# Optimization experiments

Hardware: AMD Instinct MI355X
Metric: run time of the kernel (lower is better)

## Reference

```python
import jax, jax.numpy as jnp
import numpy as np

DIM = 1028


def setup_inputs() -> dict:
    key = jax.random.key(0)
    ks = jax.random.split(key, 11)
    B, N = 8, 2048
    s = 0.02
    x = jax.random.normal(ks[0], (B, N, DIM), dtype=jnp.float32)
    Wq = jax.random.normal(ks[1], (DIM, DIM), dtype=jnp.float32) * s
    bq = jax.random.normal(ks[2], (DIM,), dtype=jnp.float32) * s
    Wk = jax.random.normal(ks[3], (DIM, DIM), dtype=jnp.float32) * s
    bk = jax.random.normal(ks[4], (DIM,), dtype=jnp.float32) * s
    Wv = jax.random.normal(ks[5], (DIM, DIM), dtype=jnp.float32) * s
    bv = jax.random.normal(ks[6], (DIM,), dtype=jnp.float32) * s
    We = jax.random.normal(ks[7], (4 * DIM, DIM), dtype=jnp.float32) * s
    be = jax.random.normal(ks[8], (4 * DIM,), dtype=jnp.float32) * s
    Wo = jax.random.normal(ks[9], (DIM, 4 * DIM), dtype=jnp.float32) * s
    bo = jax.random.normal(ks[10], (DIM,), dtype=jnp.float32) * s
    return {"x": x, "Wq": Wq, "bq": bq, "Wk": Wk, "bk": bk, "Wv": Wv,
            "bv": bv, "We": We, "be": be, "Wo": Wo, "bo": bo}


def reference(x, Wq, bq, Wk, bk, Wv, bv, We, be, Wo, bo):
    # x: [B, N, D]. torch Linear weight is [out, in] -> x @ W.T + b
    q = jnp.einsum('bnd,ed->bne', x, Wq) + bq
    k = jnp.einsum('bnd,ed->bne', x, Wk) + bk
    v = jnp.einsum('bnd,ed->bne', x, Wv) + bv
    scores = jnp.einsum('bqd,bkd->bqk', q, k) / jnp.sqrt(jnp.float32(DIM))
    w = jax.nn.softmax(scores, axis=-1)          # [B, N, N]
    attn = jnp.einsum('bqk,bkd->bqd', w, v)      # [B, N, D]
    h = jax.nn.gelu(jnp.einsum('bnd,hd->bnh', attn, We) + be, approximate=False)
    out = jnp.einsum('bnh,dh->bnd', h, Wo) + bo
    return out + x
```

## Files before the change

kernel.cpp:

```cpp
#include <hip/hip_runtime.h>
#include <hip/hip_bf16.h>
#include <cstdint>
#include <cmath>


typedef __bf16 bf16;
typedef __bf16 bf16x8 __attribute__((ext_vector_type(8)));
typedef float  f32x4  __attribute__((ext_vector_type(4)));

#define D_REAL   1028
#define D_PADK   1088
#define D_PADN   1152
#define H_REAL   4112
#define H_PAD    4224
#define NTOK     2048
#define NB       8
#define MTOT     (NB*NTOK)
#define SLAB_X   ((size_t)NTOK*D_PADK)
#define SLAB_S   ((size_t)NTOK*NTOK)
#define WSLAB    ((size_t)D_PADN*D_PADK)
#define VSLAB    ((size_t)D_PADN*NTOK)

__device__ __forceinline__ void async16(const void* g, void* l) {
    __builtin_amdgcn_global_load_lds(
        (__attribute__((address_space(1))) void*)(uintptr_t)g,
        (__attribute__((address_space(3))) void*)(uint32_t)(uintptr_t)l,
        16, 0, 0);
}

template <int EPI, bool XPIN>
__global__ __launch_bounds__(256, 2)
void gemm_bt(const bf16* __restrict__ A, size_t strideA,
             const bf16* __restrict__ B, size_t strideB,
             const float* __restrict__ bias, size_t strideBias,
             void* __restrict__ Out, size_t strideOut,
             bf16* __restrict__ OutV,
             int K, int outPitch, int colBound, float scale,
             const float* __restrict__ resid)
{
    __shared__ __attribute__((aligned(16))) bf16 tA[256 * 64];
    __shared__ __attribute__((aligned(16))) bf16 tB[128 * 64];

    int bx, by, bz;
    if (XPIN) { bz = blockIdx.x; by = blockIdx.y; bx = blockIdx.z; }
    else      { bx = blockIdx.x; by = blockIdx.y; bz = blockIdx.z; }

    A += (size_t)bz * strideA;
    B += (size_t)bz * strideB;
    if (bias) bias += (size_t)bz * strideBias;

    const int tid  = threadIdx.x;
    const int lane = tid & 63;
    const int wv   = tid >> 6;
    const int wm   = wv >> 1;
    const int wn   = wv & 1;

    f32x4 acc[8][4] = {};

    const int sRow = lane >> 3;
    const int sCh  = (lane & 7) ^ sRow;
    const bf16* gA = A + (size_t)(by * 256 + wv * 64 + sRow) * K + sCh * 8;
    const bf16* gB = B + (size_t)(bx * 128 + wv * 32 + sRow) * K + sCh * 8;
    bf16* lA = &tA[(wv * 64) * 64];
    bf16* lB = &tB[(wv * 32) * 64];

    const int lr  = lane & 15;
    const int lq  = lane >> 4;
    const int rsw = lr & 7;

    for (int k0 = 0; k0 < K; k0 += 64) {
        async16(gA,                  lA);
        async16(gA + (size_t) 8 * K, lA +  8 * 64);
        async16(gA + (size_t)16 * K, lA + 16 * 64);
        async16(gA + (size_t)24 * K, lA + 24 * 64);
        async16(gA + (size_t)32 * K, lA + 32 * 64);
        async16(gA + (size_t)40 * K, lA + 40 * 64);
        async16(gA + (size_t)48 * K, lA + 48 * 64);
        async16(gA + (size_t)56 * K, lA + 56 * 64);
        async16(gB,                  lB);
        async16(gB + (size_t) 8 * K, lB +  8 * 64);
        async16(gB + (size_t)16 * K, lB + 16 * 64);
        async16(gB + (size_t)24 * K, lB + 24 * 64);
        gA += 64; gB += 64;
        __syncthreads();

        #pragma unroll
        for (int kk = 0; kk < 2; ++kk) {
            const int sl = ((kk * 4 + lq) ^ rsw) << 3;
            bf16x8 bfr[4];
            #pragma unroll
            for (int j = 0; j < 4; ++j)
                bfr[j] = *(const bf16x8*)&tB[(wn * 64 + j * 16 + lr) * 64 + sl];
            #pragma unroll
            for (int i = 0; i < 8; ++i) {
                const bf16x8 af = *(const bf16x8*)&tA[(wm * 128 + i * 16 + lr) * 64 + sl];
                #pragma unroll
                for (int j = 0; j < 4; ++j)
                    acc[i][j] = __builtin_amdgcn_mfma_f32_16x16x32_bf16(
                        af, bfr[j], acc[i][j], 0, 0, 0);
            }
        }
        __syncthreads();
    }

    #pragma unroll
    for (int i = 0; i < 8; ++i) {
        #pragma unroll
        for (int j = 0; j < 4; ++j) {
            f32x4 v = acc[i][j];
            const int cg = bx * 128 + wn * 64 + j * 16 + lr;
            if (cg >= colBound) continue;
            const int rowBase = by * 256 + wm * 128 + i * 16 + lq * 4;
            const float bs = bias ? bias[cg] : 0.0f;
            #pragma unroll
            for (int r = 0; r < 4; ++r) {
                const int mg = rowBase + r;
                const float val = v[r];
                if (EPI == 0) {
                    ((bf16*)Out + (size_t)bz * strideOut)[(size_t)mg * outPitch + cg] =
                        (bf16)(val + bs);
                } else if (EPI == 3) {
                    const float u = val + bs;
                    const float g = 0.5f * u * (1.0f + erff(u * 0.70710678118654752f));
                    ((bf16*)Out)[(size_t)mg * outPitch + cg] = (bf16)g;
                } else if (EPI == 4) {
                    ((float*)Out)[(size_t)mg * outPitch + cg] =
                        val + bs + resid[(size_t)mg * outPitch + cg];
                } else if (EPI == 5) {
                    const int grp = cg / D_PADN;
                    const int c   = cg - grp * D_PADN;
                    const float u = val + bs;
                    if (grp < 2) {
                        if (c < D_PADK)
                            ((bf16*)Out)[(size_t)bz * 2 * SLAB_X + (size_t)grp * SLAB_X +
                                         (size_t)mg * D_PADK + c] = (bf16)u;
                    } else {
                        OutV[(size_t)bz * VSLAB + (size_t)c * NTOK + mg] = (bf16)u;
                    }
                } else {
                    ((bf16*)Out + (size_t)bz * strideOut)[(size_t)mg * outPitch + cg] =
                        (bf16)(val * scale);
                }
            }
        }
    }
}

__global__ __launch_bounds__(256)
void cvt_pad(const float* __restrict__ src, int R, int C,
             bf16* __restrict__ dst, int CP)
{
    const int c = blockIdx.x * 256 + threadIdx.x;
    const int r = blockIdx.y;
    if (c >= CP) return;
    const float v = (r < R && c < C) ? src[(size_t)r * C + c] : 0.0f;
    dst[(size_t)r * CP + c] = (bf16)v;
}

__global__ __launch_bounds__(256)
void pad_bias(const float* __restrict__ src, int n, float* __restrict__ dst, int np)
{
    const int i = blockIdx.x * 256 + threadIdx.x;
    if (i < np) dst[i] = (i < n) ? src[i] : 0.0f;
}

__global__ __launch_bounds__(256)
void softmax_ip(bf16* __restrict__ S)
{
    const int row  = blockIdx.x * 4 + (threadIdx.x >> 6);
    const int lane = threadIdx.x & 63;
    bf16* s = S + (size_t)row * NTOK + lane * 8;

    float v[32];
    #pragma unroll
    for (int j = 0; j < 4; ++j) {
        bf16x8 t = *(const bf16x8*)(s + j * 512);
        #pragma unroll
        for (int e = 0; e < 8; ++e) v[j * 8 + e] = (float)t[e];
    }
    float m = -1e30f;
    #pragma unroll
    for (int i = 0; i < 32; ++i) m = fmaxf(m, v[i]);
    #pragma unroll
    for (int off = 32; off > 0; off >>= 1) m = fmaxf(m, __shfl_xor(m, off, 64));

    float sum = 0.0f;
    #pragma unroll
    for (int i = 0; i < 32; ++i) { v[i] = __expf(v[i] - m); sum += v[i]; }
    #pragma unroll
    for (int off = 32; off > 0; off >>= 1) sum += __shfl_xor(sum, off, 64);
    const float inv = 1.0f / sum;

    #pragma unroll
    for (int j = 0; j < 4; ++j) {
        bf16x8 t;
        #pragma unroll
        for (int e = 0; e < 8; ++e) t[e] = (bf16)(v[j * 8 + e] * inv);
        *(bf16x8*)(s + j * 512) = t;
    }
}

#define OFF_WQKV   0u
#define OFF_WE     7520256u
#define OFF_WO     16711680u
#define OFF_BQKV   26443776u
#define OFF_BE     26457600u
#define OFF_XBF    26474496u
#define OFF_VT     62126080u
#define OFF_SCR    99874816u
#define QS_BYTES   8912896u
#define SS_BYTES   8388608u

extern "C" void kernel_launch(void* const* d_in, const int* in_sizes, int n_in,
                              void* d_out, int out_size, void* d_ws, size_t ws_size,
                              hipStream_t stream)
{
    const float* x  = (const float*)d_in[0];
    const float* Wq = (const float*)d_in[1];
    const float* bq = (const float*)d_in[2];
    const float* Wk = (const float*)d_in[3];
    const float* bk = (const float*)d_in[4];
    const float* Wv = (const float*)d_in[5];
    const float* bv = (const float*)d_in[6];
    const float* We = (const float*)d_in[7];
    const float* be = (const float*)d_in[8];
    const float* Wo = (const float*)d_in[9];
    const float* bo = (const float*)d_in[10];

    char* ws = (char*)d_ws;
    bf16*  Wqkv = (bf16*)(ws + OFF_WQKV);
    bf16*  WeP  = (bf16*)(ws + OFF_WE);
    bf16*  WoP  = (bf16*)(ws + OFF_WO);
    float* Bqkv = (float*)(ws + OFF_BQKV);
    float* BeP  = (float*)(ws + OFF_BE);
    bf16*  Xbf  = (bf16*)(ws + OFF_XBF);
    bf16*  Vt   = (bf16*)(ws + OFF_VT);
    char*  scr  = ws + OFF_SCR;

    const size_t avail = ws_size > OFF_SCR ? ws_size - OFF_SCR : 0;
    const size_t perG  = (size_t)QS_BYTES + SS_BYTES;
    int G = (avail >= 8 * perG) ? 8 : (avail >= 4 * perG) ? 4
          : (avail >= 2 * perG) ? 2 : 1;
    int R = (avail >= 69206016u) ? 8192 : (avail >= 34603008u) ? 4096 : 2048;

    bf16* Qs = (bf16*)scr;
    bf16* Ss = (bf16*)(scr + (size_t)G * QS_BYTES);
    bf16* Hb = (bf16*)scr;

    const dim3 blk(256);
    const float inv_sqrt_d = (float)(1.0 / sqrt((double)D_REAL));

    cvt_pad<<<dim3(5, MTOT), blk, 0, stream>>>(x, MTOT, D_REAL, Xbf, D_PADK);
    cvt_pad<<<dim3(5, D_PADN), blk, 0, stream>>>(Wq, D_REAL, D_REAL, Wqkv, D_PADK);
    cvt_pad<<<dim3(5, D_PADN), blk, 0, stream>>>(Wk, D_REAL, D_REAL, Wqkv + WSLAB, D_PADK);
    cvt_pad<<<dim3(5, D_PADN), blk, 0, stream>>>(Wv, D_REAL, D_REAL, Wqkv + 2 * WSLAB, D_PADK);
    cvt_pad<<<dim3(5, H_PAD), blk, 0, stream>>>(We, H_REAL, D_REAL, WeP, D_PADK);
    cvt_pad<<<dim3(17, D_PADN), blk, 0, stream>>>(Wo, D_REAL, H_REAL, WoP, H_PAD);
    pad_bias<<<dim3(5), blk, 0, stream>>>(bq, D_REAL, Bqkv, D_PADN);
    pad_bias<<<dim3(5), blk, 0, stream>>>(bk, D_REAL, Bqkv + D_PADN, D_PADN);
    pad_bias<<<dim3(5), blk, 0, stream>>>(bv, D_REAL, Bqkv + 2 * D_PADN, D_PADN);
    pad_bias<<<dim3(17), blk, 0, stream>>>(be, H_REAL, BeP, H_PAD);

    for (int g0 = 0; g0 < NB; g0 += G) {
        gemm_bt<5, false><<<dim3(27, 8, G), blk, 0, stream>>>(
            Xbf + (size_t)g0 * SLAB_X, SLAB_X, Wqkv, 0, Bqkv, 0,
            Qs, 0, Vt + (size_t)g0 * VSLAB,
            D_PADK, 0, 3456, 1.0f, nullptr);
        gemm_bt<6, true><<<dim3(G, 8, 16), blk, 0, stream>>>(
            Qs, 2 * SLAB_X, Qs + SLAB_X, 2 * SLAB_X, nullptr, 0,
            Ss, SLAB_S, nullptr, D_PADK, NTOK, NTOK, inv_sqrt_d, nullptr);
        softmax_ip<<<dim3(G * 512), blk, 0, stream>>>(Ss);
        gemm_bt<0, true><<<dim3(G, 8, 9), blk, 0, stream>>>(
            Ss, SLAB_S, Vt + (size_t)g0 * VSLAB, VSLAB, nullptr, 0,
            Xbf + (size_t)g0 * SLAB_X, SLAB_X, nullptr,
            NTOK, D_PADK, D_PADK, 1.0f, nullptr);
    }

    for (int r0 = 0; r0 < MTOT; r0 += R) {
        gemm_bt<3, false><<<dim3(33, R / 256, 1), blk, 0, stream>>>(
            Xbf + (size_t)r0 * D_PADK, 0, WeP, 0, BeP, 0,
            Hb, 0, nullptr, D_PADK, H_PAD, H_PAD, 1.0f, nullptr);
        gemm_bt<4, false><<<dim3(9, R / 256, 1), blk, 0, stream>>>(
            Hb, 0, WoP, 0, bo, 0,
            (float*)d_out + (size_t)r0 * D_REAL, 0, nullptr,
            H_PAD, D_REAL, D_REAL, 1.0f, x + (size_t)r0 * D_REAL);
    }
}
```

Before: 1.131 ms.

## Remap GEMM block indices for XCD-aware and chunked L2 locality

Adds a block-index remapping in the GEMM kernel. For the non-XPIN path, consecutive block IDs (which the hardware round-robins across the 8 XCDs) are assigned to contiguous tile regions per XCD. For the XPIN path, tiles are grouped into CH x CW chunks so neighbouring blocks share A/B panels in cache. The QKV grid is widened from 27 to 28 columns so the remap divides evenly, which adds extra blocks that rely on existing column bounds, and the FFN row chunk R may grow to 16384 when workspace allows.

New measurement: 1.216 ms. 7.4% more time.

```diff
diff --git a/kernel.cpp b/kernel.cpp
--- a/kernel.cpp
+++ b/kernel.cpp
@@ -36,14 +36,37 @@
              void* __restrict__ Out, size_t strideOut,
              bf16* __restrict__ OutV,
              int K, int outPitch, int colBound, float scale,
-             const float* __restrict__ resid)
+             const float* __restrict__ resid,
+             int p1, int p2, int p3)
 {
     __shared__ __attribute__((aligned(16))) bf16 tA[256 * 64];
     __shared__ __attribute__((aligned(16))) bf16 tB[128 * 64];
 
     int bx, by, bz;
-    if (XPIN) { bz = blockIdx.x; by = blockIdx.y; bx = blockIdx.z; }
-    else      { bx = blockIdx.x; by = blockIdx.y; bz = blockIdx.z; }
+    if (XPIN) {
+        bz = blockIdx.x;
+        const int ny = gridDim.y, nz = gridDim.z;
+        const int CH = p1, CW = p2;
+        const int t  = blockIdx.z * ny + blockIdx.y;
+        const int cs = CW * CH;
+        const int nchx = nz / CW;
+        const int c = t / cs, r = t % cs;
+        by = (c / nchx) * CH + (r % CH);
+        bx = (c % nchx) * CW + (r / CH);
+    } else {
+        const int nx = gridDim.x, ny = gridDim.y;
+        const int RY = p1, RX = p2, XF = p3;
+        const int orig = blockIdx.y * nx + blockIdx.x;
+        const int k = orig & 7, idx = orig >> 3;
+        const int rh = ny / RY, rw = nx / RX;
+        const int kr = k / RX, kc = k % RX;
+        int bxl, byl;
+        if (XF) { byl = idx / rw; bxl = idx % rw; }
+        else    { bxl = idx / rh; byl = idx % rh; }
+        by = kr * rh + byl;
+        bx = kc * rw + bxl;
+        bz = blockIdx.z;
+    }
 
     A += (size_t)bz * strideA;
     B += (size_t)bz * strideB;
@@ -241,7 +264,9 @@
     const size_t perG  = (size_t)QS_BYTES + SS_BYTES;
     int G = (avail >= 8 * perG) ? 8 : (avail >= 4 * perG) ? 4
           : (avail >= 2 * perG) ? 2 : 1;
-    int R = (avail >= 69206016u) ? 8192 : (avail >= 34603008u) ? 4096 : 2048;
+    int R = (avail >= 138412032u) ? 16384
+          : (avail >= 69206016u)  ? 8192
+          : (avail >= 34603008u)  ? 4096 : 2048;
 
     bf16* Qs = (bf16*)scr;
     bf16* Ss = (bf16*)(scr + (size_t)G * QS_BYTES);
@@ -262,27 +287,27 @@
     pad_bias<<<dim3(17), blk, 0, stream>>>(be, H_REAL, BeP, H_PAD);
 
     for (int g0 = 0; g0 < NB; g0 += G) {
-        gemm_bt<5, false><<<dim3(27, 8, G), blk, 0, stream>>>(
+        gemm_bt<5, false><<<dim3(28, 8, G), blk, 0, stream>>>(
             Xbf + (size_t)g0 * SLAB_X, SLAB_X, Wqkv, 0, Bqkv, 0,
             Qs, 0, Vt + (size_t)g0 * VSLAB,
-            D_PADK, 0, 3456, 1.0f, nullptr);
+            D_PADK, 0, 3456, 1.0f, nullptr, 2, 4, 0);
         gemm_bt<6, true><<<dim3(G, 8, 16), blk, 0, stream>>>(
             Qs, 2 * SLAB_X, Qs + SLAB_X, 2 * SLAB_X, nullptr, 0,
-            Ss, SLAB_S, nullptr, D_PADK, NTOK, NTOK, inv_sqrt_d, nullptr);
+            Ss, SLAB_S, nullptr, D_PADK, NTOK, NTOK, inv_sqrt_d, nullptr, 4, 4, 0);
         softmax_ip<<<dim3(G * 512), blk, 0, stream>>>(Ss);
         gemm_bt<0, true><<<dim3(G, 8, 9), blk, 0, stream>>>(
             Ss, SLAB_S, Vt + (size_t)g0 * VSLAB, VSLAB, nullptr, 0,
             Xbf + (size_t)g0 * SLAB_X, SLAB_X, nullptr,
-            NTOK, D_PADK, D_PADK, 1.0f, nullptr);
+            NTOK, D_PADK, D_PADK, 1.0f, nullptr, 2, 3, 0);
     }
 
     for (int r0 = 0; r0 < MTOT; r0 += R) {
         gemm_bt<3, false><<<dim3(33, R / 256, 1), blk, 0, stream>>>(
             Xbf + (size_t)r0 * D_PADK, 0, WeP, 0, BeP, 0,
-            Hb, 0, nullptr, D_PADK, H_PAD, H_PAD, 1.0f, nullptr);
+            Hb, 0, nullptr, D_PADK, H_PAD, H_PAD, 1.0f, nullptr, 8, 1, 1);
         gemm_bt<4, false><<<dim3(9, R / 256, 1), blk, 0, stream>>>(
             Hb, 0, WoP, 0, bo, 0,
             (float*)d_out + (size_t)r0 * D_REAL, 0, nullptr,
-            H_PAD, D_REAL, D_REAL, 1.0f, x + (size_t)r0 * D_REAL);
-    }
-}
+            H_PAD, D_REAL, D_REAL, 1.0f, x + (size_t)r0 * D_REAL, 8, 1, 1);
+    }
+}
```
